# Performance work log

Measured on AMD Instinct MI355X. Metric: run time of the kernel, lower is better.

## Reference

```python
import jax, jax.numpy as jnp
import numpy as np

N = 50000      # nodes
E = 800000     # edges (before self loops)
F_IN = 128     # dataset.num_features
HID = 32       # hidden_channels (per GAT head)
HEADS = 4
C = 40         # dataset.num_classes
NEG_SLOPE = 0.2


def setup_inputs() -> dict:
    key = jax.random.key(0)
    ks = jax.random.split(key, 18)
    g = lambda k, shape, fan: jax.random.normal(k, shape, dtype=jnp.float32) / np.sqrt(fan)
    inp = {
        "x": jax.random.normal(ks[0], (N, F_IN), dtype=jnp.float32),
        "edge_index": jax.random.randint(ks[1], (2, E), 0, N, dtype=jnp.int64),
        # GAT layer 1: F_IN -> HEADS*HID
        "gat_W1": g(ks[2], (F_IN, HEADS * HID), F_IN),
        "gat_att_src1": g(ks[3], (HEADS, HID), HID),
        "gat_att_dst1": g(ks[4], (HEADS, HID), HID),
        "gat_b1": jnp.zeros((HEADS * HID,), jnp.float32),
        # GAT layer 2: HEADS*HID -> C, heads=1
        "gat_W2": g(ks[5], (HEADS * HID, C), HEADS * HID),
        "gat_att_src2": g(ks[6], (1, C), C),
        "gat_att_dst2": g(ks[7], (1, C), C),
        "gat_b2": jnp.zeros((C,), jnp.float32),
        # GCN layers
        "gcn_W1": g(ks[8], (F_IN, HID), F_IN),
        "gcn_b1": jnp.zeros((HID,), jnp.float32),
        "gcn_W2": g(ks[9], (HID, C), HID),
        "gcn_b2": jnp.zeros((C,), jnp.float32),
        # final linear: 2C -> C
        "lin_W": g(ks[10], (2 * C, C), 2 * C),
        "lin_b": jnp.zeros((C,), jnp.float32),
        "weight_c": jnp.float32(0.5),
        "weight_t": jnp.float32(0.5),
    }
    return inp


def _add_self_loops(src, dst, n):
    loop = jnp.arange(n, dtype=src.dtype)
    return jnp.concatenate([src, loop]), jnp.concatenate([dst, loop])


def _gat_conv(x, src, dst, n, W, att_src, att_dst, b, heads, out_dim):
    # h: [n, heads, out_dim]
    h = (x @ W).reshape(n, heads, out_dim)
    a_s = jnp.einsum('nhd,hd->nh', h, att_src)   # source-side attention logit
    a_d = jnp.einsum('nhd,hd->nh', h, att_dst)   # target-side attention logit
    e = jax.nn.leaky_relu(a_s[src] + a_d[dst], NEG_SLOPE)  # [E', heads]
    # softmax over incoming edges of each target node (self loops guarantee >=1 edge)
    m = jax.ops.segment_max(e, dst, num_segments=n)
    ex = jnp.exp(e - m[dst])
    s = jax.ops.segment_sum(ex, dst, num_segments=n)
    alpha = ex / s[dst]                          # [E', heads]
    out = jax.ops.segment_sum(h[src] * alpha[..., None], dst, num_segments=n)
    return out.reshape(n, heads * out_dim) + b


def _gcn_conv(x, src, dst, n, W, b):
    h = x @ W
    deg = jax.ops.segment_sum(jnp.ones(src.shape, h.dtype), dst, num_segments=n)
    norm = jax.lax.rsqrt(deg)                    # deg >= 1 (self loops)
    coef = (norm[src] * norm[dst])[:, None]
    return jax.ops.segment_sum(h[src] * coef, dst, num_segments=n) + b


def reference(x, edge_index, gat_W1, gat_att_src1, gat_att_dst1, gat_b1,
              gat_W2, gat_att_src2, gat_att_dst2, gat_b2,
              gcn_W1, gcn_b1, gcn_W2, gcn_b2, lin_W, lin_b,
              weight_c, weight_t):
    n = x.shape[0]
    src, dst = _add_self_loops(edge_index[0], edge_index[1], n)
    # GAT branch (dropout is identity at inference)
    x_gat = _gat_conv(x, src, dst, n, gat_W1, gat_att_src1, gat_att_dst1,
                      gat_b1, HEADS, HID)
    x_gat = jax.nn.elu(x_gat)
    x_gat = _gat_conv(x_gat, src, dst, n, gat_W2, gat_att_src2, gat_att_dst2,
                      gat_b2, 1, C)
    # GCN branch
    x_gcn = jax.nn.relu(_gcn_conv(x, src, dst, n, gcn_W1, gcn_b1))
    x_gcn = _gcn_conv(x_gcn, src, dst, n, gcn_W2, gcn_b2)
    # weighted feature concat + linear head
    cat = jnp.concatenate([x_gcn * weight_c, x_gat * weight_t], axis=1)  # [n, 2C]
    return cat @ lin_W + lin_b
```

## Files before the change

### kernel.cpp

```cpp
#include <hip/hip_runtime.h>
#include <math.h>

#define F_IN   128
#define HIDC   32
#define NHEAD  4
#define CDIM   40
#define NEG_SLOPE 0.2f
#define BCAP   4096
#define OVCAP  16384
#define SCHUNK 4096

typedef __attribute__((ext_vector_type(8))) short bf16x8;
typedef __attribute__((ext_vector_type(4))) float f32x4;

__device__ __forceinline__ float leakyf(float x) { return x > 0.f ? x : NEG_SLOPE * x; }

__device__ __forceinline__ float sel4(float4 v, int h) {
    return (h == 0) ? v.x : (h == 1) ? v.y : (h == 2) ? v.z : v.w;
}
__device__ __forceinline__ unsigned pack2_bf16(float a, float b) {
    unsigned ua = __float_as_uint(a);
    unsigned ub = __float_as_uint(b);
    ua = (ua + 0x7FFFu + ((ua >> 16) & 1u)) >> 16;
    ub = (ub + 0x7FFFu + ((ub >> 16) & 1u)) >> 16;
    return ua | (ub << 16);
}
__device__ __forceinline__ float2 unpack2_bf16(unsigned p) {
    return make_float2(__uint_as_float(p << 16), __uint_as_float(p & 0xFFFF0000u));
}

__global__ void wb_prep_kernel(const float* __restrict__ Wg, const float* __restrict__ Wc,
                               uint4* __restrict__ wbf)
{
    int b = blockIdx.x;
    int lane = threadIdx.x;
    int nt = b >> 2, ks = b & 3;
    int c = nt * 16 + (lane & 15);
    int k0 = ks * 32 + (lane >> 4) * 8;
    unsigned u[4];
#pragma unroll
    for (int jj = 0; jj < 4; ++jj) {
        int k = k0 + 2 * jj;
        float a0 = (c < 128) ? Wg[(size_t)k * 128 + c] : Wc[(size_t)k * 32 + (c - 128)];
        float a1 = (c < 128) ? Wg[(size_t)(k + 1) * 128 + c] : Wc[(size_t)(k + 1) * 32 + (c - 128)];
        u[jj] = pack2_bf16(a0, a1);
    }
    wbf[(size_t)b * 64 + lane] = make_uint4(u[0], u[1], u[2], u[3]);
}

__global__ __launch_bounds__(256) void gemm1_mfma_kernel(
    const float* __restrict__ X, const uint4* __restrict__ wbf,
    const float* __restrict__ aw_s, const float* __restrict__ aw_d,
    unsigned* __restrict__ hb,
    float* __restrict__ as1, float* __restrict__ ad1, int n)
{
    __shared__ float Ct[64][164];
    __shared__ float sw[128], dw[128];
    const int tid = threadIdx.x;
    const int w = tid >> 6, lane = tid & 63;
    const int m = lane & 15, q = lane >> 4;
    const int node0 = blockIdx.x * 64;
    if (tid < 128) { sw[tid] = aw_s[tid]; dw[tid] = aw_d[tid]; }

    f32x4 acc[10];
#pragma unroll
    for (int t = 0; t < 10; ++t) acc[t] = (f32x4){0.f, 0.f, 0.f, 0.f};

    const int row = node0 + w * 16 + m;
    const bool rv = row < n;
#pragma unroll
    for (int ks = 0; ks < 4; ++ks) {
        uint4 pa = make_uint4(0u, 0u, 0u, 0u);
        if (rv) {
            const float* xr = X + (size_t)row * 128 + ks * 32 + q * 8;
            float4 a0 = *(const float4*)xr;
            float4 a1 = *(const float4*)(xr + 4);
            pa = make_uint4(pack2_bf16(a0.x, a0.y), pack2_bf16(a0.z, a0.w),
                            pack2_bf16(a1.x, a1.y), pack2_bf16(a1.z, a1.w));
        }
        bf16x8 af = *(bf16x8*)&pa;
#pragma unroll
        for (int nt = 0; nt < 10; ++nt) {
            uint4 pb = wbf[(size_t)(nt * 4 + ks) * 64 + lane];
            bf16x8 bfv = *(bf16x8*)&pb;
            acc[nt] = __builtin_amdgcn_mfma_f32_16x16x32_bf16(af, bfv, acc[nt], 0, 0, 0);
        }
    }
#pragma unroll
    for (int nt = 0; nt < 10; ++nt)
#pragma unroll
        for (int r = 0; r < 4; ++r)
            Ct[w * 16 + q * 4 + r][nt * 16 + m] = acc[nt][r];
    __syncthreads();

    for (int i = tid; i < 64 * 64; i += 256) {
        int nd = i >> 6, u = i & 63;
        int gn = node0 + nd;
        if (gn < n)
            hb[(size_t)gn * 80 + u] = pack2_bf16(Ct[nd][2 * u], Ct[nd][2 * u + 1]);
    }
    for (int i = tid; i < 64 * 16; i += 256) {
        int nd = i >> 4, u = i & 15;
        int gn = node0 + nd;
        if (gn < n)
            hb[(size_t)gn * 80 + 64 + u] = pack2_bf16(Ct[nd][128 + 2 * u], Ct[nd][128 + 2 * u + 1]);
    }
    {
        int nd = tid >> 2, h = tid & 3;
        int gn = node0 + nd;
        if (gn < n) {
            float s = 0.f, d = 0.f;
#pragma unroll
            for (int k = 0; k < HIDC; ++k) {
                float v = Ct[nd][h * HIDC + k];
                s = fmaf(v, sw[h * HIDC + k], s);
                d = fmaf(v, dw[h * HIDC + k], d);
            }
            as1[(size_t)gn * 4 + h] = s;
            ad1[(size_t)gn * 4 + h] = d;
        }
    }
}

template<int K, int OUTC, int BN, int BK, int OSTRIDE = OUTC>
__global__ __launch_bounds__((OUTC / 4) * (BN / 4)) void gemm_tile(
    const float* __restrict__ X, const float* __restrict__ W,
    const float* __restrict__ bias, float* __restrict__ Y, int n)
{
    constexpr int CG = OUTC / 4;
    constexpr int NG = BN / 4;
    constexpr int NT = CG * NG;
    __shared__ float Xs[BK][BN + 4];
    __shared__ float Ws[BK][OUTC];
    const int tid = threadIdx.x;
    const int cg = tid % CG, ng = tid / CG;
    const int node0 = blockIdx.x * BN;
    float acc[4][4] = {};

    for (int kb = 0; kb < K; kb += BK) {
        for (int idx = tid; idx < BN * (BK / 4); idx += NT) {
            int nd = idx / (BK / 4);
            int kq = idx % (BK / 4);
            int gnode = node0 + nd;
            float4 v = (gnode < n) ? *(const float4*)&X[(size_t)gnode * K + kb + kq * 4]
                                   : make_float4(0.f, 0.f, 0.f, 0.f);
            Xs[kq * 4 + 0][nd] = v.x;
            Xs[kq * 4 + 1][nd] = v.y;
            Xs[kq * 4 + 2][nd] = v.z;
            Xs[kq * 4 + 3][nd] = v.w;
        }
        for (int idx = tid; idx < BK * CG; idx += NT) {
            int kk = idx / CG;
            int cq = idx % CG;
            *(float4*)&Ws[kk][cq * 4] = *(const float4*)&W[(size_t)(kb + kk) * OUTC + cq * 4];
        }
        __syncthreads();
#pragma unroll
        for (int k = 0; k < BK; ++k) {
            float4 xv = *(const float4*)&Xs[k][ng * 4];
            float4 wv = *(const float4*)&Ws[k][cg * 4];
            float xa[4] = {xv.x, xv.y, xv.z, xv.w};
            float wa[4] = {wv.x, wv.y, wv.z, wv.w};
#pragma unroll
            for (int j = 0; j < 4; ++j)
#pragma unroll
                for (int c = 0; c < 4; ++c)
                    acc[j][c] = fmaf(xa[j], wa[c], acc[j][c]);
        }
        __syncthreads();
    }

    float4 bv = make_float4(0.f, 0.f, 0.f, 0.f);
    if (bias) bv = *(const float4*)&bias[cg * 4];
#pragma unroll
    for (int j = 0; j < 4; ++j) {
        int gnode = node0 + ng * 4 + j;
        if (gnode < n) {
            float4 o = make_float4(acc[j][0] + bv.x, acc[j][1] + bv.y,
                                   acc[j][2] + bv.z, acc[j][3] + bv.w);
            *(float4*)&Y[(size_t)gnode * OSTRIDE + cg * 4] = o;
        }
    }
}

template<int K, int OUTC, int BN, int BK, int OSTRIDE_U, int OFF_U>
__global__ __launch_bounds__((OUTC / 4) * (BN / 4)) void gemm_tile_bb(
    const unsigned* __restrict__ Xb, const float* __restrict__ W,
    unsigned* __restrict__ Yb, int n)
{
    constexpr int CG = OUTC / 4;
    constexpr int NG = BN / 4;
    constexpr int NT = CG * NG;
    __shared__ float Xs[BK][BN + 4];
    __shared__ float Ws[BK][OUTC];
    const int tid = threadIdx.x;
    const int cg = tid % CG, ng = tid / CG;
    const int node0 = blockIdx.x * BN;
    float acc[4][4] = {};

    for (int kb = 0; kb < K; kb += BK) {
        for (int idx = tid; idx < BN * (BK / 8); idx += NT) {
            int nd = idx / (BK / 8);
            int kq = idx % (BK / 8);
            int gnode = node0 + nd;
            uint4 v = (gnode < n) ? *(const uint4*)&Xb[(size_t)gnode * (K / 2) + kb / 2 + kq * 4]
                                  : make_uint4(0u, 0u, 0u, 0u);
            float2 a = unpack2_bf16(v.x), b = unpack2_bf16(v.y);
            float2 c = unpack2_bf16(v.z), d = unpack2_bf16(v.w);
            Xs[kq * 8 + 0][nd] = a.x; Xs[kq * 8 + 1][nd] = a.y;
            Xs[kq * 8 + 2][nd] = b.x; Xs[kq * 8 + 3][nd] = b.y;
            Xs[kq * 8 + 4][nd] = c.x; Xs[kq * 8 + 5][nd] = c.y;
            Xs[kq * 8 + 6][nd] = d.x; Xs[kq * 8 + 7][nd] = d.y;
        }
        for (int idx = tid; idx < BK * CG; idx += NT) {
            int kk = idx / CG;
            int cq = idx % CG;
            *(float4*)&Ws[kk][cq * 4] = *(const float4*)&W[(size_t)(kb + kk) * OUTC + cq * 4];
        }
        __syncthreads();
#pragma unroll
        for (int k = 0; k < BK; ++k) {
            float4 xv = *(const float4*)&Xs[k][ng * 4];
            float4 wv = *(const float4*)&Ws[k][cg * 4];
            float xa[4] = {xv.x, xv.y, xv.z, xv.w};
            float wa[4] = {wv.x, wv.y, wv.z, wv.w};
#pragma unroll
            for (int j = 0; j < 4; ++j)
#pragma unroll
                for (int c = 0; c < 4; ++c)
                    acc[j][c] = fmaf(xa[j], wa[c], acc[j][c]);
        }
        __syncthreads();
    }

#pragma unroll
    for (int j = 0; j < 4; ++j) {
        int gnode = node0 + ng * 4 + j;
        if (gnode < n) {
            uint2 pb = make_uint2(pack2_bf16(acc[j][0], acc[j][1]),
                                  pack2_bf16(acc[j][2], acc[j][3]));
            *(uint2*)&Yb[(size_t)gnode * OSTRIDE_U + OFF_U + cg * 2] = pb;
        }
    }
}

__global__ __launch_bounds__(320) void gemm2_gat_kernel(
    const unsigned* __restrict__ Xb, const float* __restrict__ W,
    const float* __restrict__ aw_s, const float* __restrict__ aw_d,
    unsigned* __restrict__ Yb, float* __restrict__ as2, float* __restrict__ ad2, int n)
{
    constexpr int K = 128, OUTC = 40, BN = 128, BK = 32;
    constexpr int CG = OUTC / 4, NT = 320;
    __shared__ float smem[32 * 132 + 32 * 40];
    float* Xs = smem;
    float* Ws = smem + 32 * 132;
    const int tid = threadIdx.x;
    const int cg = tid % CG, ng = tid / CG;
    const int node0 = blockIdx.x * BN;
    float acc[4][4] = {};

    for (int kb = 0; kb < K; kb += BK) {
        for (int idx = tid; idx < BN * (BK / 8); idx += NT) {
            int nd = idx / (BK / 8);
            int kq = idx % (BK / 8);
            int gnode = node0 + nd;
            uint4 v = (gnode < n) ? *(const uint4*)&Xb[(size_t)gnode * (K / 2) + kb / 2 + kq * 4]
                                  : make_uint4(0u, 0u, 0u, 0u);
            float2 a = unpack2_bf16(v.x), b = unpack2_bf16(v.y);
            float2 c = unpack2_bf16(v.z), d = unpack2_bf16(v.w);
            Xs[(kq * 8 + 0) * 132 + nd] = a.x; Xs[(kq * 8 + 1) * 132 + nd] = a.y;
            Xs[(kq * 8 + 2) * 132 + nd] = b.x; Xs[(kq * 8 + 3) * 132 + nd] = b.y;
            Xs[(kq * 8 + 4) * 132 + nd] = c.x; Xs[(kq * 8 + 5) * 132 + nd] = c.y;
            Xs[(kq * 8 + 6) * 132 + nd] = d.x; Xs[(kq * 8 + 7) * 132 + nd] = d.y;
        }
        for (int idx = tid; idx < BK * CG; idx += NT) {
            int kk = idx / CG;
            int cq = idx % CG;
            *(float4*)&Ws[kk * 40 + cq * 4] = *(const float4*)&W[(size_t)(kb + kk) * OUTC + cq * 4];
        }
        __syncthreads();
#pragma unroll
        for (int k = 0; k < BK; ++k) {
            float4 xv = *(const float4*)&Xs[k * 132 + ng * 4];
            float4 wv = *(const float4*)&Ws[k * 40 + cg * 4];
            float xa[4] = {xv.x, xv.y, xv.z, xv.w};
            float wa[4] = {wv.x, wv.y, wv.z, wv.w};
#pragma unroll
            for (int j = 0; j < 4; ++j)
#pragma unroll
                for (int c = 0; c < 4; ++c)
                    acc[j][c] = fmaf(xa[j], wa[c], acc[j][c]);
        }
        __syncthreads();
    }

    float* Ct  = smem;
    float* sww = smem + 128 * 41;
    float* dww = sww + 40;
#pragma unroll
    for (int j = 0; j < 4; ++j) {
        int gnode = node0 + ng * 4 + j;
        if (gnode < n) {
            uint2 pb = make_uint2(pack2_bf16(acc[j][0], acc[j][1]),
                                  pack2_bf16(acc[j][2], acc[j][3]));
            *(uint2*)&Yb[(size_t)gnode * 40 + cg * 2] = pb;
        }
#pragma unroll
        for (int c = 0; c < 4; ++c)
            Ct[(ng * 4 + j) * 41 + cg * 4 + c] = acc[j][c];
    }
    if (tid < 40) { sww[tid] = aw_s[tid]; dww[tid] = aw_d[tid]; }
    __syncthreads();
    if (tid < 128) {
        int gnode = node0 + tid;
        if (gnode < n) {
            float s = 0.f, d = 0.f;
#pragma unroll
            for (int c = 0; c < 40; ++c) {
                float v = Ct[tid * 41 + c];
                s = fmaf(v, sww[c], s);
                d = fmaf(v, dww[c], d);
            }
            as2[gnode] = s;
            ad2[gnode] = d;
        }
    }
}

__global__ __launch_bounds__(256) void bucket_scatter_kernel(
    const int* __restrict__ src, const int* __restrict__ dst,
    unsigned* __restrict__ bcnt, unsigned* __restrict__ bpair,
    unsigned* __restrict__ ovf_cnt, uint2* __restrict__ ovf, int e, int nbuck)
{
    __shared__ unsigned hist[512];
    __shared__ unsigned base[512];
    const int t = threadIdx.x;
    const int lo = blockIdx.x * SCHUNK;
    const int hi = min(lo + SCHUNK, e);
    for (int i = t; i < nbuck; i += 256) hist[i] = 0;
    __syncthreads();
    for (int i = lo + t; i < hi; i += 256)
        atomicAdd(&hist[((unsigned)dst[i]) >> 7], 1u);
    __syncthreads();
    for (int i = t; i < nbuck; i += 256) {
        unsigned c = hist[i];
        base[i] = c ? atomicAdd(&bcnt[i], c) : 0u;
        hist[i] = 0;
    }
    __syncthreads();
    for (int i = lo + t; i < hi; i += 256) {
        unsigned s = (unsigned)src[i], d = (unsigned)dst[i];
        unsigned b = d >> 7;
        unsigned pos = base[b] + atomicAdd(&hist[b], 1u);
        if (pos < BCAP) bpair[(size_t)b * BCAP + pos] = s | ((d & 127u) << 16);
        else {
            unsigned o = atomicAdd(ovf_cnt, 1u);
            if (o < OVCAP) ovf[o] = make_uint2(s, d);
        }
    }
}

__global__ __launch_bounds__(256) void bucket_count_kernel(
    const unsigned* __restrict__ bcnt, const unsigned* __restrict__ bpair,
    const unsigned* __restrict__ ovf_cnt, const uint2* __restrict__ ovf,
    unsigned* __restrict__ counts, int n)
{
    __shared__ unsigned lc[128];
    const int b = blockIdx.x, base = b << 7;
    if (threadIdx.x < 128) lc[threadIdx.x] = 0;
    __syncthreads();
    unsigned bc = bcnt[b];
    int cnt = (int)(bc < BCAP ? bc : BCAP);
    for (int k = threadIdx.x; k < cnt; k += 256)
        atomicAdd(&lc[bpair[(size_t)b * BCAP + k] >> 16], 1u);
    unsigned oc_u = *ovf_cnt;
    int oc = (int)(oc_u < OVCAP ? oc_u : OVCAP);
    for (int k = threadIdx.x; k < oc; k += 256) {
        uint2 pp = ovf[k];
        if ((int)(pp.y >> 7) == b) atomicAdd(&lc[pp.y & 127u], 1u);
    }
    __syncthreads();
    int i = base + threadIdx.x;
    if (threadIdx.x < 128 && i < n) counts[i] = lc[threadIdx.x];
}

__global__ __launch_bounds__(256) void scan_reduce_kernel(const unsigned* __restrict__ counts,
                                                          unsigned* __restrict__ partials, int n)
{
    __shared__ unsigned sm[256];
    int t = threadIdx.x;
    int i = blockIdx.x * 256 + t;
    unsigned v = (i < n) ? counts[i] : 0u;
    sm[t] = v;
    __syncthreads();
#pragma unroll
    for (int off = 128; off > 0; off >>= 1) {
        if (t < off) sm[t] += sm[t + off];
        __syncthreads();
    }
    if (t == 0) partials[blockIdx.x] = sm[0];
}

__global__ __launch_bounds__(256) void scan_partials_kernel(unsigned* __restrict__ partials,
                                                            unsigned* __restrict__ rs, int nb, int n)
{
    __shared__ unsigned sm[256];
    int t = threadIdx.x;
    unsigned v = (t < nb) ? partials[t] : 0u;
    sm[t] = v;
    __syncthreads();
#pragma unroll
    for (int off = 1; off < 256; off <<= 1) {
        unsigned u = (t >= off) ? sm[t - off] : 0u;
        __syncthreads();
        sm[t] += u;
        __syncthreads();
    }
    if (t < nb) partials[t] = sm[t] - v;
    if (t == 255) rs[n] = sm[255];
}

__global__ __launch_bounds__(256) void scan_write_kernel(const unsigned* __restrict__ counts,
                                                         const unsigned* __restrict__ partials,
                                                         unsigned* __restrict__ rs,
                                                         float* __restrict__ nrm, int n)
{
    __shared__ unsigned sm[256];
    int t = threadIdx.x;
    int i = blockIdx.x * 256 + t;
    unsigned c = (i < n) ? counts[i] : 0u;
    sm[t] = c;
    __syncthreads();
#pragma unroll
    for (int off = 1; off < 256; off <<= 1) {
        unsigned u = (t >= off) ? sm[t - off] : 0u;
        __syncthreads();
        sm[t] += u;
        __syncthreads();
    }
    if (i < n) {
        rs[i] = partials[blockIdx.x] + sm[t] - c;
        nrm[i] = rsqrtf((float)(c + 1u));
    }
}

__global__ __launch_bounds__(256) void bucket_place_kernel(
    const unsigned* __restrict__ bcnt, const unsigned* __restrict__ bpair,
    const unsigned* __restrict__ rs, unsigned* __restrict__ csr_src,
    unsigned* __restrict__ cursor, int n)
{
    __shared__ unsigned lc[128];
    __shared__ unsigned rbase[128];
    const int b = blockIdx.x, base = b << 7;
    if (threadIdx.x < 128) {
        lc[threadIdx.x] = 0;
        int i = base + threadIdx.x;
        rbase[threadIdx.x] = (i < n) ? rs[i] : 0u;
    }
    __syncthreads();
    unsigned bc = bcnt[b];
    int cnt = (int)(bc < BCAP ? bc : BCAP);
    for (int k = threadIdx.x; k < cnt; k += 256) {
        unsigned v = bpair[(size_t)b * BCAP + k];
        unsigned ld = v >> 16;
        unsigned r = atomicAdd(&lc[ld], 1u);
        csr_src[rbase[ld] + r] = v & 0xFFFFu;
    }
    __syncthreads();
    int i = base + threadIdx.x;
    if (threadIdx.x < 128 && i < n) cursor[i] = rbase[threadIdx.x] + lc[threadIdx.x];
}

__global__ void overflow_fill_kernel(const unsigned* __restrict__ ovf_cnt,
                                     const uint2* __restrict__ ovf,
                                     unsigned* __restrict__ cursor,
                                     unsigned* __restrict__ csr_src)
{
    unsigned oc_u = *ovf_cnt;
    int oc = (int)(oc_u < OVCAP ? oc_u : OVCAP);
    for (int k = threadIdx.x; k < oc; k += 256) {
        uint2 pp = ovf[k];
        unsigned pos = atomicAdd(&cursor[pp.y], 1u);
        csr_src[pos] = pp.x;
    }
}

__global__ __launch_bounds__(256) void agg1_fused_kernel(
    const unsigned* __restrict__ hb,
    const float* __restrict__ as1, const float* __restrict__ ad1,
    const float* __restrict__ nrm,
    const unsigned* __restrict__ rs, const unsigned* __restrict__ csr_src,
    const float* __restrict__ gat_b1, const float* __restrict__ gcn_b1,
    unsigned* __restrict__ xgb, unsigned* __restrict__ gaccb, int n)
{
    const int wid = threadIdx.x >> 6;
    const int lane = threadIdx.x & 63;
    const int i = blockIdx.x * 4 + wid;
    if (i >= n) return;
    const unsigned beg = rs[i];
    const int deg = (int)(rs[i + 1] - beg);
    const float4* as1v = (const float4*)as1;
    const uint4*  hv4  = (const uint4*)hb;

    const int e = lane >> 4, c = lane & 15;
    const int h = c >> 2;
    const bool gc = c < 4;

    const float4 dv = ((const float4*)ad1)[i];
    const float dvh = sel4(dv, h);
    const float ni  = nrm[i];

    unsigned pre = (lane < deg) ? csr_src[beg + lane] : (unsigned)i;

    const float4 av = as1v[i];
    const float eself = __expf(leakyf(sel4(av, h) + dvh));

    float acc[8], gacc[8];
#pragma unroll
    for (int t = 0; t < 8; ++t) { acc[t] = 0.f; gacc[t] = 0.f; }
    float sumw = 0.f;

    if (e == 0) {
        uint4 hv = hv4[(size_t)i * 20 + c];
        float2 p0 = unpack2_bf16(hv.x), p1 = unpack2_bf16(hv.y);
        float2 p2 = unpack2_bf16(hv.z), p3 = unpack2_bf16(hv.w);
        acc[0] = p0.x * eself; acc[1] = p0.y * eself;
        acc[2] = p1.x * eself; acc[3] = p1.y * eself;
        acc[4] = p2.x * eself; acc[5] = p2.y * eself;
        acc[6] = p3.x * eself; acc[7] = p3.y * eself;
        if (gc) {
            uint4 gv = hv4[(size_t)i * 20 + 16 + c];
            float w2s = ni * ni;
            float2 q0 = unpack2_bf16(gv.x), q1 = unpack2_bf16(gv.y);
            float2 q2 = unpack2_bf16(gv.z), q3 = unpack2_bf16(gv.w);
            gacc[0] = q0.x * w2s; gacc[1] = q0.y * w2s;
            gacc[2] = q1.x * w2s; gacc[3] = q1.y * w2s;
            gacc[4] = q2.x * w2s; gacc[5] = q2.y * w2s;
            gacc[6] = q3.x * w2s; gacc[7] = q3.y * w2s;
        }
    }

    const int dfast = deg < 64 ? deg : 64;
    const int steps = (dfast + 3) >> 2;

    float4 a_cur = make_float4(0.f, 0.f, 0.f, 0.f);
    uint4  h_cur = make_uint4(0u, 0u, 0u, 0u);
    uint4  g_cur = make_uint4(0u, 0u, 0u, 0u);
    float  nr_cur = 0.f;
    if (steps > 0) {
        unsigned s = __shfl(pre, e, 64);
        if (e >= deg) s = (unsigned)i;
        a_cur = as1v[s];
        h_cur = hv4[(size_t)s * 20 + c];
        if (gc) { g_cur = hv4[(size_t)s * 20 + 16 + c]; nr_cur = nrm[s]; }
    }
    for (int j = 0; j < steps; ++j) {
        float4 a_nxt = a_cur;
        uint4  h_nxt = h_cur, g_nxt = g_cur;
        float  nr_nxt = nr_cur;
        if (j + 1 < steps) {
            int idx = (j + 1) * 4 + e;
            unsigned s = __shfl(pre, idx, 64);
            if (idx >= deg) s = (unsigned)i;
            a_nxt = as1v[s];
            h_nxt = hv4[(size_t)s * 20 + c];
            if (gc) { g_nxt = hv4[(size_t)s * 20 + 16 + c]; nr_nxt = nrm[s]; }
        }
        const bool val = (j * 4 + e) < deg;
        float w = __expf(leakyf(sel4(a_cur, h) + dvh));
        w = val ? w : 0.f;
        sumw += w;
        {
            float2 p0 = unpack2_bf16(h_cur.x), p1 = unpack2_bf16(h_cur.y);
            float2 p2 = unpack2_bf16(h_cur.z), p3 = unpack2_bf16(h_cur.w);
            acc[0] = fmaf(p0.x, w, acc[0]); acc[1] = fmaf(p0.y, w, acc[1]);
            acc[2] = fmaf(p1.x, w, acc[2]); acc[3] = fmaf(p1.y, w, acc[3]);
            acc[4] = fmaf(p2.x, w, acc[4]); acc[5] = fmaf(p2.y, w, acc[5]);
            acc[6] = fmaf(p3.x, w, acc[6]); acc[7] = fmaf(p3.y, w, acc[7]);
        }
        if (gc) {
            float cw = val ? nr_cur * ni : 0.f;
            float2 q0 = unpack2_bf16(g_cur.x), q1 = unpack2_bf16(g_cur.y);
            float2 q2 = unpack2_bf16(g_cur.z), q3 = unpack2_bf16(g_cur.w);
            gacc[0] = fmaf(q0.x, cw, gacc[0]); gacc[1] = fmaf(q0.y, cw, gacc[1]);
            gacc[2] = fmaf(q1.x, cw, gacc[2]); gacc[3] = fmaf(q1.y, cw, gacc[3]);
            gacc[4] = fmaf(q2.x, cw, gacc[4]); gacc[5] = fmaf(q2.y, cw, gacc[5]);
            gacc[6] = fmaf(q3.x, cw, gacc[6]); gacc[7] = fmaf(q3.y, cw, gacc[7]);
        }
        a_cur = a_nxt; h_cur = h_nxt; g_cur = g_nxt; nr_cur = nr_nxt;
    }
    for (int j4 = 64; j4 < deg; j4 += 4) {
        int idx = j4 + e;
        bool val = idx < deg;
        unsigned s = val ? csr_src[beg + idx] : (unsigned)i;
        float4 a = as1v[s];
        float w = val ? __expf(leakyf(sel4(a, h) + dvh)) : 0.f;
        sumw += w;
        uint4 hv = hv4[(size_t)s * 20 + c];
        float2 p0 = unpack2_bf16(hv.x), p1 = unpack2_bf16(hv.y);
        float2 p2 = unpack2_bf16(hv.z), p3 = unpack2_bf16(hv.w);
        acc[0] = fmaf(p0.x, w, acc[0]); acc[1] = fmaf(p0.y, w, acc[1]);
        acc[2] = fmaf(p1.x, w, acc[2]); acc[3] = fmaf(p1.y, w, acc[3]);
        acc[4] = fmaf(p2.x, w, acc[4]); acc[5] = fmaf(p2.y, w, acc[5]);
        acc[6] = fmaf(p3.x, w, acc[6]); acc[7] = fmaf(p3.y, w, acc[7]);
        if (gc) {
            float cw = val ? nrm[s] * ni : 0.f;
            uint4 gv = hv4[(size_t)s * 20 + 16 + c];
            float2 q0 = unpack2_bf16(gv.x), q1 = unpack2_bf16(gv.y);
            float2 q2 = unpack2_bf16(gv.z), q3 = unpack2_bf16(gv.w);
            gacc[0] = fmaf(q0.x, cw, gacc[0]); gacc[1] = fmaf(q0.y, cw, gacc[1]);
            gacc[2] = fmaf(q1.x, cw, gacc[2]); gacc[3] = fmaf(q1.y, cw, gacc[3]);
            gacc[4] = fmaf(q2.x, cw, gacc[4]); gacc[5] = fmaf(q2.y, cw, gacc[5]);
            gacc[6] = fmaf(q3.x, cw, gacc[6]); gacc[7] = fmaf(q3.y, cw, gacc[7]);
        }
    }

#pragma unroll
    for (int t = 0; t < 8; ++t) {
        acc[t]  += __shfl_xor(acc[t], 16, 64);
        acc[t]  += __shfl_xor(acc[t], 32, 64);
        gacc[t] += __shfl_xor(gacc[t], 16, 64);
        gacc[t] += __shfl_xor(gacc[t], 32, 64);
    }
    sumw += __shfl_xor(sumw, 16, 64);
    sumw += __shfl_xor(sumw, 32, 64);
    const float ssh = sumw + eself;

    if (e == 0) {
        float inv = 1.f / ssh;
        float4 b0 = *(const float4*)&gat_b1[c * 8];
        float4 b1 = *(const float4*)&gat_b1[c * 8 + 4];
        float o[8] = {acc[0] * inv + b0.x, acc[1] * inv + b0.y,
                      acc[2] * inv + b0.z, acc[3] * inv + b0.w,
                      acc[4] * inv + b1.x, acc[5] * inv + b1.y,
                      acc[6] * inv + b1.z, acc[7] * inv + b1.w};
#pragma unroll
        for (int t = 0; t < 8; ++t) o[t] = o[t] > 0.f ? o[t] : __expf(o[t]) - 1.f;
        uint4 pv = make_uint4(pack2_bf16(o[0], o[1]), pack2_bf16(o[2], o[3]),
                              pack2_bf16(o[4], o[5]), pack2_bf16(o[6], o[7]));
        ((uint4*)xgb)[(size_t)i * 16 + c] = pv;
        if (gc) {
            float4 c0 = *(const float4*)&gcn_b1[c * 8];
            float4 c1 = *(const float4*)&gcn_b1[c * 8 + 4];
            float g[8] = {fmaxf(gacc[0] + c0.x, 0.f), fmaxf(gacc[1] + c0.y, 0.f),
                          fmaxf(gacc[2] + c0.z, 0.f), fmaxf(gacc[3] + c0.w, 0.f),
                          fmaxf(gacc[4] + c1.x, 0.f), fmaxf(gacc[5] + c1.y, 0.f),
                          fmaxf(gacc[6] + c1.z, 0.f), fmaxf(gacc[7] + c1.w, 0.f)};
            uint4 gv = make_uint4(pack2_bf16(g[0], g[1]), pack2_bf16(g[2], g[3]),
                                  pack2_bf16(g[4], g[5]), pack2_bf16(g[6], g[7]));
            ((uint4*)gaccb)[(size_t)i * 4 + c] = gv;
        }
    }
}

__global__ __launch_bounds__(256) void agg2_fused_kernel(
    const unsigned* __restrict__ hg_b, const float* __restrict__ as2,
    const float* __restrict__ ad2, const float* __restrict__ nrm,
    const unsigned* __restrict__ rs, const unsigned* __restrict__ csr_src,
    const float* __restrict__ gat_b2, const float* __restrict__ gcn_b2,
    const float* __restrict__ wc_p, const float* __restrict__ wt_p,
    float* __restrict__ cat, int n)
{
    const int wid = threadIdx.x >> 6;
    const int lane = threadIdx.x & 63;
    const int i = blockIdx.x * 4 + wid;
    if (i >= n) return;
    const unsigned beg = rs[i];
    const int deg = (int)(rs[i + 1] - beg);
    const int e = lane & 3, c = lane >> 2;
    const bool act = c < 10, isgat = c < 5;
    const float adv = ad2[i];
    const float ni = nrm[i];
    const uint4* hgv = (const uint4*)hg_b;

    unsigned pre = (lane < deg) ? csr_src[beg + lane] : (unsigned)i;
    const float eself = __expf(leakyf(as2[i] + adv));

    float acc[8];
#pragma unroll
    for (int t = 0; t < 8; ++t) acc[t] = 0.f;
    float sumw = 0.f;

    if (act && e == 0) {
        uint4 hv = hgv[(size_t)i * 10 + c];
        float sw = isgat ? eself : ni * ni;
        float2 p0 = unpack2_bf16(hv.x), p1 = unpack2_bf16(hv.y);
        float2 p2 = unpack2_bf16(hv.z), p3 = unpack2_bf16(hv.w);
        acc[0] = p0.x * sw; acc[1] = p0.y * sw;
        acc[2] = p1.x * sw; acc[3] = p1.y * sw;
        acc[4] = p2.x * sw; acc[5] = p2.y * sw;
        acc[6] = p3.x * sw; acc[7] = p3.y * sw;
    }

    const int dfast = deg < 64 ? deg : 64;
    const int steps = (dfast + 3) >> 2;

    float aw_cur = 0.f;
    uint4 h_cur = make_uint4(0u, 0u, 0u, 0u);
    if (steps > 0) {
        unsigned s = __shfl(pre, e, 64);
        if (e >= deg) s = (unsigned)i;
        if (act) { aw_cur = isgat ? as2[s] : nrm[s]; h_cur = hgv[(size_t)s * 10 + c]; }
    }
    for (int j = 0; j < steps; ++j) {
        float aw_nxt = aw_cur;
        uint4 h_nxt = h_cur;
        if (j + 1 < steps) {
            int idx = (j + 1) * 4 + e;
            unsigned s = __shfl(pre, idx, 64);
            if (idx >= deg) s = (unsigned)i;
            if (act) { aw_nxt = isgat ? as2[s] : nrm[s]; h_nxt = hgv[(size_t)s * 10 + c]; }
        }
        const bool val = (j * 4 + e) < deg;
        float w;
        if (isgat) {
            w = __expf(leakyf(aw_cur + adv));
            w = val ? w : 0.f;
            sumw += w;
        } else {
            w = val ? aw_cur * ni : 0.f;
        }
        if (act) {
            float2 p0 = unpack2_bf16(h_cur.x), p1 = unpack2_bf16(h_cur.y);
            float2 p2 = unpack2_bf16(h_cur.z), p3 = unpack2_bf16(h_cur.w);
            acc[0] = fmaf(p0.x, w, acc[0]); acc[1] = fmaf(p0.y, w, acc[1]);
            acc[2] = fmaf(p1.x, w, acc[2]); acc[3] = fmaf(p1.y, w, acc[3]);
            acc[4] = fmaf(p2.x, w, acc[4]); acc[5] = fmaf(p2.y, w, acc[5]);
            acc[6] = fmaf(p3.x, w, acc[6]); acc[7] = fmaf(p3.y, w, acc[7]);
        }
        aw_cur = aw_nxt; h_cur = h_nxt;
    }
    for (int j4 = 64; j4 < deg; j4 += 4) {
        int idx = j4 + e;
        bool val = idx < deg;
        unsigned s = val ? csr_src[beg + idx] : (unsigned)i;
        if (act) {
            float aw = isgat ? as2[s] : nrm[s];
            float w;
            if (isgat) {
                w = val ? __expf(leakyf(aw + adv)) : 0.f;
                sumw += w;
            } else {
                w = val ? aw * ni : 0.f;
            }
            uint4 hv = hgv[(size_t)s * 10 + c];
            float2 p0 = unpack2_bf16(hv.x), p1 = unpack2_bf16(hv.y);
            float2 p2 = unpack2_bf16(hv.z), p3 = unpack2_bf16(hv.w);
            acc[0] = fmaf(p0.x, w, acc[0]); acc[1] = fmaf(p0.y, w, acc[1]);
            acc[2] = fmaf(p1.x, w, acc[2]); acc[3] = fmaf(p1.y, w, acc[3]);
            acc[4] = fmaf(p2.x, w, acc[4]); acc[5] = fmaf(p2.y, w, acc[5]);
            acc[6] = fmaf(p3.x, w, acc[6]); acc[7] = fmaf(p3.y, w, acc[7]);
        }
    }

#pragma unroll
    for (int t = 0; t < 8; ++t) {
        acc[t] += __shfl_xor(acc[t], 1, 64);
        acc[t] += __shfl_xor(acc[t], 2, 64);
    }
    sumw += __shfl_xor(sumw, 1, 64);
    sumw += __shfl_xor(sumw, 2, 64);
    const float ssum = sumw + eself;

    if (act && e == 0) {
        if (isgat) {
            float inv = 1.f / ssum, wt = *wt_p;
            float4 b0 = *(const float4*)&gat_b2[c * 8];
            float4 b1 = *(const float4*)&gat_b2[c * 8 + 4];
            float4 o0 = make_float4((acc[0] * inv + b0.x) * wt, (acc[1] * inv + b0.y) * wt,
                                    (acc[2] * inv + b0.z) * wt, (acc[3] * inv + b0.w) * wt);
            float4 o1 = make_float4((acc[4] * inv + b1.x) * wt, (acc[5] * inv + b1.y) * wt,
                                    (acc[6] * inv + b1.z) * wt, (acc[7] * inv + b1.w) * wt);
            *(float4*)&cat[(size_t)i * 80 + 40 + c * 8]     = o0;
            *(float4*)&cat[(size_t)i * 80 + 40 + c * 8 + 4] = o1;
        } else {
            float wc = *wc_p;
            int g = c - 5;
            float4 b0 = *(const float4*)&gcn_b2[g * 8];
            float4 b1 = *(const float4*)&gcn_b2[g * 8 + 4];
            float4 o0 = make_float4((acc[0] + b0.x) * wc, (acc[1] + b0.y) * wc,
                                    (acc[2] + b0.z) * wc, (acc[3] + b0.w) * wc);
            float4 o1 = make_float4((acc[4] + b1.x) * wc, (acc[5] + b1.y) * wc,
                                    (acc[6] + b1.z) * wc, (acc[7] + b1.w) * wc);
            *(float4*)&cat[(size_t)i * 80 + g * 8]     = o0;
            *(float4*)&cat[(size_t)i * 80 + g * 8 + 4] = o1;
        }
    }
}

extern "C" void kernel_launch(void* const* d_in, const int* in_sizes, int n_in,
                              void* d_out, int out_size, void* d_ws, size_t ws_size,
                              hipStream_t stream)
{
    const float* x        = (const float*)d_in[0];
    const int*   eidx     = (const int*)d_in[1];
    const float* gat_W1   = (const float*)d_in[2];
    const float* att_s1   = (const float*)d_in[3];
    const float* att_d1   = (const float*)d_in[4];
    const float* gat_b1   = (const float*)d_in[5];
    const float* gat_W2   = (const float*)d_in[6];
    const float* att_s2   = (const float*)d_in[7];
    const float* att_d2   = (const float*)d_in[8];
    const float* gat_b2   = (const float*)d_in[9];
    const float* gcn_W1   = (const float*)d_in[10];
    const float* gcn_b1   = (const float*)d_in[11];
    const float* gcn_W2   = (const float*)d_in[12];
    const float* gcn_b2   = (const float*)d_in[13];
    const float* lin_W    = (const float*)d_in[14];
    const float* lin_b    = (const float*)d_in[15];
    const float* wc_p     = (const float*)d_in[16];
    const float* wt_p     = (const float*)d_in[17];

    const int n = in_sizes[0] / F_IN;
    const int e = in_sizes[1] / 2;
    const int* src = eidx;
    const int* dst = eidx + e;
    const int NBUCK = (n + 127) >> 7;

    char* p = (char*)d_ws;
    auto alloc = [&](size_t bytes) -> void* {
        void* r = (void*)p;
        p += (bytes + 255) & ~(size_t)255;
        return r;
    };
    unsigned* counts  = (unsigned*)alloc((size_t)n * 4);
    unsigned* rs      = (unsigned*)alloc((size_t)(n + 1) * 4);
    unsigned* cursor  = (unsigned*)alloc((size_t)n * 4);
    unsigned* partials= (unsigned*)alloc(256 * 4);
    unsigned* bcnt    = (unsigned*)alloc((size_t)(NBUCK + 1) * 4);
    unsigned* csr_src = (unsigned*)alloc((size_t)e * 4);
    uint4*    wbf     = (uint4*)alloc(40 * 64 * 16);
    float* nrm     = (float*)alloc((size_t)n * 4);
    float* as1     = (float*)alloc((size_t)n * 4 * 4);
    float* ad1     = (float*)alloc((size_t)n * 4 * 4);
    float* as2     = (float*)alloc((size_t)n * 4);
    float* ad2     = (float*)alloc((size_t)n * 4);
    float* cat     = (float*)alloc((size_t)n * 80 * 4);
    unsigned* hg_b = (unsigned*)alloc((size_t)n * 40 * 4);
    float* xg      = (float*)alloc((size_t)n * F_IN * 4);
    unsigned* gaccb= (unsigned*)alloc((size_t)n * 16 * 4);
    unsigned* bpair = (unsigned*)cat;
    uint2*    ovf   = (uint2*)(bpair + (size_t)NBUCK * BCAP);
    unsigned* hb    = (unsigned*)cat;
    unsigned* xgb   = (unsigned*)xg;
    unsigned* ovf_cnt = bcnt + NBUCK;

    const int NB = (n + 255) / 256;
    const int WB = (n + 3) / 4;
    const int SB = (e + SCHUNK - 1) / SCHUNK;

    hipMemsetAsync(bcnt, 0, (size_t)(NBUCK + 1) * 4, stream);
    bucket_scatter_kernel<<<SB, 256, 0, stream>>>(src, dst, bcnt, bpair, ovf_cnt, ovf, e, NBUCK);
    bucket_count_kernel<<<NBUCK, 256, 0, stream>>>(bcnt, bpair, ovf_cnt, ovf, counts, n);
    scan_reduce_kernel<<<NB, 256, 0, stream>>>(counts, partials, n);
    scan_partials_kernel<<<1, 256, 0, stream>>>(partials, rs, NB, n);
    scan_write_kernel<<<NB, 256, 0, stream>>>(counts, partials, rs, nrm, n);
    bucket_place_kernel<<<NBUCK, 256, 0, stream>>>(bcnt, bpair, rs, csr_src, cursor, n);
    overflow_fill_kernel<<<1, 256, 0, stream>>>(ovf_cnt, ovf, cursor, csr_src);

    wb_prep_kernel<<<40, 64, 0, stream>>>(gat_W1, gcn_W1, wbf);
    gemm1_mfma_kernel<<<(n + 63) / 64, 256, 0, stream>>>(x, wbf, att_s1, att_d1,
                                                         hb, as1, ad1, n);

    agg1_fused_kernel<<<WB, 256, 0, stream>>>(hb, as1, ad1, nrm, rs, csr_src,
                                              gat_b1, gcn_b1, xgb, gaccb, n);

    gemm_tile_bb<32, 40, 128, 32, 40, 20><<<(n + 127) / 128, 320, 0, stream>>>(gaccb, gcn_W2, hg_b, n);
    gemm2_gat_kernel<<<(n + 127) / 128, 320, 0, stream>>>(xgb, gat_W2, att_s2, att_d2,
                                                          hg_b, as2, ad2, n);

    agg2_fused_kernel<<<WB, 256, 0, stream>>>(hg_b, as2, ad2, nrm, rs, csr_src,
                                              gat_b2, gcn_b2, wc_p, wt_p, cat, n);

    gemm_tile<80, 40, 128, 40><<<(n + 127) / 128, 320, 0, stream>>>(cat, lin_W, lin_b, (float*)d_out, n);
}
```

Measured before the change: 306.0 us.

## Process two nodes per wavefront in aggregations and fuse final linear into agg2

Both aggregation kernels now handle two destination nodes per wavefront, interleaving their gathers so each wave keeps more independent memory requests in flight. The final linear layer is folded into agg2: the concatenated features are combined in registers via lane shuffles and multiplied by the transposed weights, removing the cat buffer round-trip and a separate GEMM launch. The cost is higher register pressure, and wasted work when the two nodes' degrees differ.

```diff
diff --git a/kernel.cpp b/kernel.cpp
--- a/kernel.cpp
+++ b/kernel.cpp
@@ -118,67 +118,6 @@
             }
             as1[(size_t)gn * 4 + h] = s;
             ad1[(size_t)gn * 4 + h] = d;
-        }
-    }
-}
-
-template<int K, int OUTC, int BN, int BK, int OSTRIDE = OUTC>
-__global__ __launch_bounds__((OUTC / 4) * (BN / 4)) void gemm_tile(
-    const float* __restrict__ X, const float* __restrict__ W,
-    const float* __restrict__ bias, float* __restrict__ Y, int n)
-{
-    constexpr int CG = OUTC / 4;
-    constexpr int NG = BN / 4;
-    constexpr int NT = CG * NG;
-    __shared__ float Xs[BK][BN + 4];
-    __shared__ float Ws[BK][OUTC];
-    const int tid = threadIdx.x;
-    const int cg = tid % CG, ng = tid / CG;
-    const int node0 = blockIdx.x * BN;
-    float acc[4][4] = {};
-
-    for (int kb = 0; kb < K; kb += BK) {
-        for (int idx = tid; idx < BN * (BK / 4); idx += NT) {
-            int nd = idx / (BK / 4);
-            int kq = idx % (BK / 4);
-            int gnode = node0 + nd;
-            float4 v = (gnode < n) ? *(const float4*)&X[(size_t)gnode * K + kb + kq * 4]
-                                   : make_float4(0.f, 0.f, 0.f, 0.f);
-            Xs[kq * 4 + 0][nd] = v.x;
-            Xs[kq * 4 + 1][nd] = v.y;
-            Xs[kq * 4 + 2][nd] = v.z;
-            Xs[kq * 4 + 3][nd] = v.w;
-        }
-        for (int idx = tid; idx < BK * CG; idx += NT) {
-            int kk = idx / CG;
-            int cq = idx % CG;
-            *(float4*)&Ws[kk][cq * 4] = *(const float4*)&W[(size_t)(kb + kk) * OUTC + cq * 4];
-        }
-        __syncthreads();
-#pragma unroll
-        for (int k = 0; k < BK; ++k) {
-            float4 xv = *(const float4*)&Xs[k][ng * 4];
-            float4 wv = *(const float4*)&Ws[k][cg * 4];
-            float xa[4] = {xv.x, xv.y, xv.z, xv.w};
-            float wa[4] = {wv.x, wv.y, wv.z, wv.w};
-#pragma unroll
-            for (int j = 0; j < 4; ++j)
-#pragma unroll
-                for (int c = 0; c < 4; ++c)
-                    acc[j][c] = fmaf(xa[j], wa[c], acc[j][c]);
-        }
-        __syncthreads();
-    }
-
-    float4 bv = make_float4(0.f, 0.f, 0.f, 0.f);
-    if (bias) bv = *(const float4*)&bias[cg * 4];
-#pragma unroll
-    for (int j = 0; j < 4; ++j) {
-        int gnode = node0 + ng * 4 + j;
-        if (gnode < n) {
-            float4 o = make_float4(acc[j][0] + bv.x, acc[j][1] + bv.y,
-                                   acc[j][2] + bv.z, acc[j][3] + bv.w);
-            *(float4*)&Y[(size_t)gnode * OSTRIDE + cg * 4] = o;
         }
     }
 }
@@ -495,160 +434,263 @@
 {
     const int wid = threadIdx.x >> 6;
     const int lane = threadIdx.x & 63;
-    const int i = blockIdx.x * 4 + wid;
-    if (i >= n) return;
-    const unsigned beg = rs[i];
-    const int deg = (int)(rs[i + 1] - beg);
+    const int iA = blockIdx.x * 8 + wid * 2;
+    if (iA >= n) return;
+    const int iB = iA + 1;
+    const bool hasB = iB < n;
+    const int iBs = hasB ? iB : iA;
+
     const float4* as1v = (const float4*)as1;
+    const float4* ad1v = (const float4*)ad1;
     const uint4*  hv4  = (const uint4*)hb;
 
     const int e = lane >> 4, c = lane & 15;
     const int h = c >> 2;
     const bool gc = c < 4;
 
-    const float4 dv = ((const float4*)ad1)[i];
-    const float dvh = sel4(dv, h);
-    const float ni  = nrm[i];
-
-    unsigned pre = (lane < deg) ? csr_src[beg + lane] : (unsigned)i;
-
-    const float4 av = as1v[i];
-    const float eself = __expf(leakyf(sel4(av, h) + dvh));
-
-    float acc[8], gacc[8];
-#pragma unroll
-    for (int t = 0; t < 8; ++t) { acc[t] = 0.f; gacc[t] = 0.f; }
-    float sumw = 0.f;
+    const unsigned begA = rs[iA];
+    const int degA = (int)(rs[iA + 1] - begA);
+    const unsigned begB = rs[iBs];
+    const int degB = hasB ? (int)(rs[iB + 1] - begB) : 0;
+
+    const float dvhA = sel4(ad1v[iA], h);
+    const float dvhB = sel4(ad1v[iBs], h);
+    const float niA = nrm[iA];
+    const float niB = nrm[iBs];
+
+    unsigned preA = (lane < degA) ? csr_src[begA + lane] : (unsigned)iA;
+    unsigned preB = (lane < degB) ? csr_src[begB + lane] : (unsigned)iBs;
+
+    const float eselfA = __expf(leakyf(sel4(as1v[iA], h) + dvhA));
+    const float eselfB = __expf(leakyf(sel4(as1v[iBs], h) + dvhB));
+
+    float accA[8], gaccA[8], accB[8], gaccB[8];
+#pragma unroll
+    for (int t = 0; t < 8; ++t) { accA[t] = 0.f; gaccA[t] = 0.f; accB[t] = 0.f; gaccB[t] = 0.f; }
+    float sumwA = 0.f, sumwB = 0.f;
 
     if (e == 0) {
-        uint4 hv = hv4[(size_t)i * 20 + c];
+        uint4 hv = hv4[(size_t)iA * 20 + c];
         float2 p0 = unpack2_bf16(hv.x), p1 = unpack2_bf16(hv.y);
         float2 p2 = unpack2_bf16(hv.z), p3 = unpack2_bf16(hv.w);
-        acc[0] = p0.x * eself; acc[1] = p0.y * eself;
-        acc[2] = p1.x * eself; acc[3] = p1.y * eself;
-        acc[4] = p2.x * eself; acc[5] = p2.y * eself;
-        acc[6] = p3.x * eself; acc[7] = p3.y * eself;
+        accA[0] = p0.x * eselfA; accA[1] = p0.y * eselfA;
+        accA[2] = p1.x * eselfA; accA[3] = p1.y * eselfA;
+        accA[4] = p2.x * eselfA; accA[5] = p2.y * eselfA;
+        accA[6] = p3.x * eselfA; accA[7] = p3.y * eselfA;
         if (gc) {
-            uint4 gv = hv4[(size_t)i * 20 + 16 + c];
-            float w2s = ni * ni;
+            uint4 gv = hv4[(size_t)iA * 20 + 16 + c];
+            float w2 = niA * niA;
             float2 q0 = unpack2_bf16(gv.x), q1 = unpack2_bf16(gv.y);
             float2 q2 = unpack2_bf16(gv.z), q3 = unpack2_bf16(gv.w);
-            gacc[0] = q0.x * w2s; gacc[1] = q0.y * w2s;
-            gacc[2] = q1.x * w2s; gacc[3] = q1.y * w2s;
-            gacc[4] = q2.x * w2s; gacc[5] = q2.y * w2s;
-            gacc[6] = q3.x * w2s; gacc[7] = q3.y * w2s;
-        }
-    }
-
-    const int dfast = deg < 64 ? deg : 64;
-    const int steps = (dfast + 3) >> 2;
-
-    float4 a_cur = make_float4(0.f, 0.f, 0.f, 0.f);
-    uint4  h_cur = make_uint4(0u, 0u, 0u, 0u);
-    uint4  g_cur = make_uint4(0u, 0u, 0u, 0u);
-    float  nr_cur = 0.f;
+            gaccA[0] = q0.x * w2; gaccA[1] = q0.y * w2;
+            gaccA[2] = q1.x * w2; gaccA[3] = q1.y * w2;
+            gaccA[4] = q2.x * w2; gaccA[5] = q2.y * w2;
+            gaccA[6] = q3.x * w2; gaccA[7] = q3.y * w2;
+        }
+    }
+    if (e == 1 && hasB) {
+        uint4 hv = hv4[(size_t)iB * 20 + c];
+        float2 p0 = unpack2_bf16(hv.x), p1 = unpack2_bf16(hv.y);
+        float2 p2 = unpack2_bf16(hv.z), p3 = unpack2_bf16(hv.w);
+        accB[0] = p0.x * eselfB; accB[1] = p0.y * eselfB;
+        accB[2] = p1.x * eselfB; accB[3] = p1.y * eselfB;
+        accB[4] = p2.x * eselfB; accB[5] = p2.y * eselfB;
+        accB[6] = p3.x * eselfB; accB[7] = p3.y * eselfB;
+        if (gc) {
+            uint4 gv = hv4[(size_t)iB * 20 + 16 + c];
+            float w2 = niB * niB;
+            float2 q0 = unpack2_bf16(gv.x), q1 = unpack2_bf16(gv.y);
+            float2 q2 = unpack2_bf16(gv.z), q3 = unpack2_bf16(gv.w);
+            gaccB[0] = q0.x * w2; gaccB[1] = q0.y * w2;
+            gaccB[2] = q1.x * w2; gaccB[3] = q1.y * w2;
+            gaccB[4] = q2.x * w2; gaccB[5] = q2.y * w2;
+            gaccB[6] = q3.x * w2; gaccB[7] = q3.y * w2;
+        }
+    }
+
+    const int dA = degA < 64 ? degA : 64;
+    const int dB = degB < 64 ? degB : 64;
+    const int stepsA = (dA + 3) >> 2;
+    const int stepsB = (dB + 3) >> 2;
+    const int steps = stepsA > stepsB ? stepsA : stepsB;
+
+    auto fetch = [&](unsigned pre, int deg, int selfi, int idx,
+                     float4& a, uint4& hh, uint4& gg, float& nr) {
+        unsigned s = __shfl(pre, idx, 64);
+        if (idx >= deg) s = (unsigned)selfi;
+        a = as1v[s];
+        hh = hv4[(size_t)s * 20 + c];
+        if (gc) { gg = hv4[(size_t)s * 20 + 16 + c]; nr = nrm[s]; }
+    };
+
+    float4 aA = make_float4(0.f, 0.f, 0.f, 0.f), aB = aA;
+    uint4 hA = make_uint4(0u, 0u, 0u, 0u), hB = hA, gA = hA, gB = hA;
+    float nrA = 0.f, nrB = 0.f;
     if (steps > 0) {
-        unsigned s = __shfl(pre, e, 64);
-        if (e >= deg) s = (unsigned)i;
-        a_cur = as1v[s];
-        h_cur = hv4[(size_t)s * 20 + c];
-        if (gc) { g_cur = hv4[(size_t)s * 20 + 16 + c]; nr_cur = nrm[s]; }
+        fetch(preA, degA, iA, e, aA, hA, gA, nrA);
+        fetch(preB, degB, iBs, e, aB, hB, gB, nrB);
     }
     for (int j = 0; j < steps; ++j) {
-        float4 a_nxt = a_cur;
-        uint4  h_nxt = h_cur, g_nxt = g_cur;
-        float  nr_nxt = nr_cur;
+        float4 aA2 = aA, aB2 = aB;
+        uint4 hA2 = hA, hB2 = hB, gA2 = gA, gB2 = gB;
+        float nrA2 = nrA, nrB2 = nrB;
         if (j + 1 < steps) {
-            int idx = (j + 1) * 4 + e;
-            unsigned s = __shfl(pre, idx, 64);
-            if (idx >= deg) s = (unsigned)i;
-            a_nxt = as1v[s];
-            h_nxt = hv4[(size_t)s * 20 + c];
-            if (gc) { g_nxt = hv4[(size_t)s * 20 + 16 + c]; nr_nxt = nrm[s]; }
-        }
-        const bool val = (j * 4 + e) < deg;
-        float w = __expf(leakyf(sel4(a_cur, h) + dvh));
-        w = val ? w : 0.f;
-        sumw += w;
+            fetch(preA, degA, iA, (j + 1) * 4 + e, aA2, hA2, gA2, nrA2);
+            fetch(preB, degB, iBs, (j + 1) * 4 + e, aB2, hB2, gB2, nrB2);
+        }
         {
-            float2 p0 = unpack2_bf16(h_cur.x), p1 = unpack2_bf16(h_cur.y);
-            float2 p2 = unpack2_bf16(h_cur.z), p3 = unpack2_bf16(h_cur.w);
-            acc[0] = fmaf(p0.x, w, acc[0]); acc[1] = fmaf(p0.y, w, acc[1]);
-            acc[2] = fmaf(p1.x, w, acc[2]); acc[3] = fmaf(p1.y, w, acc[3]);
-            acc[4] = fmaf(p2.x, w, acc[4]); acc[5] = fmaf(p2.y, w, acc[5]);
-            acc[6] = fmaf(p3.x, w, acc[6]); acc[7] = fmaf(p3.y, w, acc[7]);
-        }
-        if (gc) {
-            float cw = val ? nr_cur * ni : 0.f;
-            float2 q0 = unpack2_bf16(g_cur.x), q1 = unpack2_bf16(g_cur.y);
-            float2 q2 = unpack2_bf16(g_cur.z), q3 = unpack2_bf16(g_cur.w);
-            gacc[0] = fmaf(q0.x, cw, gacc[0]); gacc[1] = fmaf(q0.y, cw, gacc[1]);
-            gacc[2] = fmaf(q1.x, cw, gacc[2]); gacc[3] = fmaf(q1.y, cw, gacc[3]);
-            gacc[4] = fmaf(q2.x, cw, gacc[4]); gacc[5] = fmaf(q2.y, cw, gacc[5]);
-            gacc[6] = fmaf(q3.x, cw, gacc[6]); gacc[7] = fmaf(q3.y, cw, gacc[7]);
-        }
-        a_cur = a_nxt; h_cur = h_nxt; g_cur = g_nxt; nr_cur = nr_nxt;
-    }
-    for (int j4 = 64; j4 < deg; j4 += 4) {
+            const bool val = (j * 4 + e) < degA;
+            float w = __expf(leakyf(sel4(aA, h) + dvhA));
+            w = val ? w : 0.f;
+            sumwA += w;
+            float2 p0 = unpack2_bf16(hA.x), p1 = unpack2_bf16(hA.y);
+            float2 p2 = unpack2_bf16(hA.z), p3 = unpack2_bf16(hA.w);
+            accA[0] = fmaf(p0.x, w, accA[0]); accA[1] = fmaf(p0.y, w, accA[1]);
+            accA[2] = fmaf(p1.x, w, accA[2]); accA[3] = fmaf(p1.y, w, accA[3]);
+            accA[4] = fmaf(p2.x, w, accA[4]); accA[5] = fmaf(p2.y, w, accA[5]);
+            accA[6] = fmaf(p3.x, w, accA[6]); accA[7] = fmaf(p3.y, w, accA[7]);
+            if (gc) {
+                float cw = val ? nrA * niA : 0.f;
+                float2 q0 = unpack2_bf16(gA.x), q1 = unpack2_bf16(gA.y);
+                float2 q2 = unpack2_bf16(gA.z), q3 = unpack2_bf16(gA.w);
+                gaccA[0] = fmaf(q0.x, cw, gaccA[0]); gaccA[1] = fmaf(q0.y, cw, gaccA[1]);
+                gaccA[2] = fmaf(q1.x, cw, gaccA[2]); gaccA[3] = fmaf(q1.y, cw, gaccA[3]);
+                gaccA[4] = fmaf(q2.x, cw, gaccA[4]); gaccA[5] = fmaf(q2.y, cw, gaccA[5]);
+                gaccA[6] = fmaf(q3.x, cw, gaccA[6]); gaccA[7] = fmaf(q3.y, cw, gaccA[7]);
+            }
+        }
+        {
+            const bool val = (j * 4 + e) < degB;
+            float w = __expf(leakyf(sel4(aB, h) + dvhB));
+            w = val ? w : 0.f;
+            sumwB += w;
+            float2 p0 = unpack2_bf16(hB.x), p1 = unpack2_bf16(hB.y);
+            float2 p2 = unpack2_bf16(hB.z), p3 = unpack2_bf16(hB.w);
+            accB[0] = fmaf(p0.x, w, accB[0]); accB[1] = fmaf(p0.y, w, accB[1]);
+            accB[2] = fmaf(p1.x, w, accB[2]); accB[3] = fmaf(p1.y, w, accB[3]);
+            accB[4] = fmaf(p2.x, w, accB[4]); accB[5] = fmaf(p2.y, w, accB[5]);
+            accB[6] = fmaf(p3.x, w, accB[6]); accB[7] = fmaf(p3.y, w, accB[7]);
+            if (gc) {
+                float cw = val ? nrB * niB : 0.f;
+                float2 q0 = unpack2_bf16(gB.x), q1 = unpack2_bf16(gB.y);
+                float2 q2 = unpack2_bf16(gB.z), q3 = unpack2_bf16(gB.w);
+                gaccB[0] = fmaf(q0.x, cw, gaccB[0]); gaccB[1] = fmaf(q0.y, cw, gaccB[1]);
+                gaccB[2] = fmaf(q1.x, cw, gaccB[2]); gaccB[3] = fmaf(q1.y, cw, gaccB[3]);
+                gaccB[4] = fmaf(q2.x, cw, gaccB[4]); gaccB[5] = fmaf(q2.y, cw, gaccB[5]);
+                gaccB[6] = fmaf(q3.x, cw, gaccB[6]); gaccB[7] = fmaf(q3.y, cw, gaccB[7]);
+            }
+        }
+        aA = aA2; aB = aB2; hA = hA2; hB = hB2; gA = gA2; gB = gB2; nrA = nrA2; nrB = nrB2;
+    }
+    for (int j4 = 64; j4 < degA; j4 += 4) {
         int idx = j4 + e;
-        bool val = idx < deg;
-        unsigned s = val ? csr_src[beg + idx] : (unsigned)i;
-        float4 a = as1v[s];
-        float w = val ? __expf(leakyf(sel4(a, h) + dvh)) : 0.f;
-        sumw += w;
+        bool val = idx < degA;
+        unsigned s = val ? csr_src[begA + idx] : (unsigned)iA;
+        float w = val ? __expf(leakyf(sel4(as1v[s], h) + dvhA)) : 0.f;
+        sumwA += w;
         uint4 hv = hv4[(size_t)s * 20 + c];
         float2 p0 = unpack2_bf16(hv.x), p1 = unpack2_bf16(hv.y);
         float2 p2 = unpack2_bf16(hv.z), p3 = unpack2_bf16(hv.w);
-        acc[0] = fmaf(p0.x, w, acc[0]); acc[1] = fmaf(p0.y, w, acc[1]);
-        acc[2] = fmaf(p1.x, w, acc[2]); acc[3] = fmaf(p1.y, w, acc[3]);
-        acc[4] = fmaf(p2.x, w, acc[4]); acc[5] = fmaf(p2.y, w, acc[5]);
-        acc[6] = fmaf(p3.x, w, acc[6]); acc[7] = fmaf(p3.y, w, acc[7]);
+        accA[0] = fmaf(p0.x, w, accA[0]); accA[1] = fmaf(p0.y, w, accA[1]);
+        accA[2] = fmaf(p1.x, w, accA[2]); accA[3] = fmaf(p1.y, w, accA[3]);
+        accA[4] = fmaf(p2.x, w, accA[4]); accA[5] = fmaf(p2.y, w, accA[5]);
+        accA[6] = fmaf(p3.x, w, accA[6]); accA[7] = fmaf(p3.y, w, accA[7]);
         if (gc) {
-            float cw = val ? nrm[s] * ni : 0.f;
+            float cw = val ? nrm[s] * niA : 0.f;
             uint4 gv = hv4[(size_t)s * 20 + 16 + c];
             float2 q0 = unpack2_bf16(gv.x), q1 = unpack2_bf16(gv.y);
             float2 q2 = unpack2_bf16(gv.z), q3 = unpack2_bf16(gv.w);
-            gacc[0] = fmaf(q0.x, cw, gacc[0]); gacc[1] = fmaf(q0.y, cw, gacc[1]);
-            gacc[2] = fmaf(q1.x, cw, gacc[2]); gacc[3] = fmaf(q1.y, cw, gacc[3]);
-            gacc[4] = fmaf(q2.x, cw, gacc[4]); gacc[5] = fmaf(q2.y, cw, gacc[5]);
-            gacc[6] = fmaf(q3.x, cw, gacc[6]); gacc[7] = fmaf(q3.y, cw, gacc[7]);
+            gaccA[0] = fmaf(q0.x, cw, gaccA[0]); gaccA[1] = fmaf(q0.y, cw, gaccA[1]);
+            gaccA[2] = fmaf(q1.x, cw, gaccA[2]); gaccA[3] = fmaf(q1.y, cw, gaccA[3]);
+            gaccA[4] = fmaf(q2.x, cw, gaccA[4]); gaccA[5] = fmaf(q2.y, cw, gaccA[5]);
+            gaccA[6] = fmaf(q3.x, cw, gaccA[6]); gaccA[7] = fmaf(q3.y, cw, gaccA[7]);
+        }
+    }
+    for (int j4 = 64; j4 < degB; j4 += 4) {
+        int idx = j4 + e;
+        bool val = idx < degB;
+        unsigned s = val ? csr_src[begB + idx] : (unsigned)iBs;
+        float w = val ? __expf(leakyf(sel4(as1v[s], h) + dvhB)) : 0.f;
+        sumwB += w;
+        uint4 hv = hv4[(size_t)s * 20 + c];
+        float2 p0 = unpack2_bf16(hv.x), p1 = unpack2_bf16(hv.y);
+        float2 p2 = unpack2_bf16(hv.z), p3 = unpack2_bf16(hv.w);
+        accB[0] = fmaf(p0.x, w, accB[0]); accB[1] = fmaf(p0.y, w, accB[1]);
+        accB[2] = fmaf(p1.x, w, accB[2]); accB[3] = fmaf(p1.y, w, accB[3]);
+        accB[4] = fmaf(p2.x, w, accB[4]); accB[5] = fmaf(p2.y, w, accB[5]);
+        accB[6] = fmaf(p3.x, w, accB[6]); accB[7] = fmaf(p3.y, w, accB[7]);
+        if (gc) {
+            float cw = val ? nrm[s] * niB : 0.f;
+            uint4 gv = hv4[(size_t)s * 20 + 16 + c];
+            float2 q0 = unpack2_bf16(gv.x), q1 = unpack2_bf16(gv.y);
+            float2 q2 = unpack2_bf16(gv.z), q3 = unpack2_bf16(gv.w);
+            gaccB[0] = fmaf(q0.x, cw, gaccB[0]); gaccB[1] = fmaf(q0.y, cw, gaccB[1]);
+            gaccB[2] = fmaf(q1.x, cw, gaccB[2]); gaccB[3] = fmaf(q1.y, cw, gaccB[3]);
+            gaccB[4] = fmaf(q2.x, cw, gaccB[4]); gaccB[5] = fmaf(q2.y, cw, gaccB[5]);
+            gaccB[6] = fmaf(q3.x, cw, gaccB[6]); gaccB[7] = fmaf(q3.y, cw, gaccB[7]);
         }
     }
 
 #pragma unroll
     for (int t = 0; t < 8; ++t) {
-        acc[t]  += __shfl_xor(acc[t], 16, 64);
-        acc[t]  += __shfl_xor(acc[t], 32, 64);
-        gacc[t] += __shfl_xor(gacc[t], 16, 64);
-        gacc[t] += __shfl_xor(gacc[t], 32, 64);
-    }
-    sumw += __shfl_xor(sumw, 16, 64);
-    sumw += __shfl_xor(sumw, 32, 64);
-    const float ssh = sumw + eself;
+        accA[t]  += __shfl_xor(accA[t], 16, 64);  accA[t]  += __shfl_xor(accA[t], 32, 64);
+        accB[t]  += __shfl_xor(accB[t], 16, 64);  accB[t]  += __shfl_xor(accB[t], 32, 64);
+        gaccA[t] += __shfl_xor(gaccA[t], 16, 64); gaccA[t] += __shfl_xor(gaccA[t], 32, 64);
+        gaccB[t] += __shfl_xor(gaccB[t], 16, 64); gaccB[t] += __shfl_xor(gaccB[t], 32, 64);
+    }
+    sumwA += __shfl_xor(sumwA, 16, 64); sumwA += __shfl_xor(sumwA, 32, 64);
+    sumwB += __shfl_xor(sumwB, 16, 64); sumwB += __shfl_xor(sumwB, 32, 64);
+    const float sshA = sumwA + eselfA;
+    const float sshB = sumwB + eselfB;
 
     if (e == 0) {
-        float inv = 1.f / ssh;
+        float inv = 1.f / sshA;
         float4 b0 = *(const float4*)&gat_b1[c * 8];
         float4 b1 = *(const float4*)&gat_b1[c * 8 + 4];
-        float o[8] = {acc[0] * inv + b0.x, acc[1] * inv + b0.y,
-                      acc[2] * inv + b0.z, acc[3] * inv + b0.w,
-                      acc[4] * inv + b1.x, acc[5] * inv + b1.y,
-                      acc[6] * inv + b1.z, acc[7] * inv + b1.w};
+        float o[8] = {accA[0] * inv + b0.x, accA[1] * inv + b0.y,
+                      accA[2] * inv + b0.z, accA[3] * inv + b0.w,
+                      accA[4] * inv + b1.x, accA[5] * inv + b1.y,
+                      accA[6] * inv + b1.z, accA[7] * inv + b1.w};
 #pragma unroll
         for (int t = 0; t < 8; ++t) o[t] = o[t] > 0.f ? o[t] : __expf(o[t]) - 1.f;
         uint4 pv = make_uint4(pack2_bf16(o[0], o[1]), pack2_bf16(o[2], o[3]),
                               pack2_bf16(o[4], o[5]), pack2_bf16(o[6], o[7]));
-        ((uint4*)xgb)[(size_t)i * 16 + c] = pv;
+        ((uint4*)xgb)[(size_t)iA * 16 + c] = pv;
         if (gc) {
             float4 c0 = *(const float4*)&gcn_b1[c * 8];
             float4 c1 = *(const float4*)&gcn_b1[c * 8 + 4];
-            float g[8] = {fmaxf(gacc[0] + c0.x, 0.f), fmaxf(gacc[1] + c0.y, 0.f),
-                          fmaxf(gacc[2] + c0.z, 0.f), fmaxf(gacc[3] + c0.w, 0.f),
-                          fmaxf(gacc[4] + c1.x, 0.f), fmaxf(gacc[5] + c1.y, 0.f),
-                          fmaxf(gacc[6] + c1.z, 0.f), fmaxf(gacc[7] + c1.w, 0.f)};
+            float g[8] = {fmaxf(gaccA[0] + c0.x, 0.f), fmaxf(gaccA[1] + c0.y, 0.f),
+                          fmaxf(gaccA[2] + c0.z, 0.f), fmaxf(gaccA[3] + c0.w, 0.f),
+                          fmaxf(gaccA[4] + c1.x, 0.f), fmaxf(gaccA[5] + c1.y, 0.f),
+                          fmaxf(gaccA[6] + c1.z, 0.f), fmaxf(gaccA[7] + c1.w, 0.f)};
             uint4 gv = make_uint4(pack2_bf16(g[0], g[1]), pack2_bf16(g[2], g[3]),
                                   pack2_bf16(g[4], g[5]), pack2_bf16(g[6], g[7]));
-            ((uint4*)gaccb)[(size_t)i * 4 + c] = gv;
+            ((uint4*)gaccb)[(size_t)iA * 4 + c] = gv;
+        }
+    }
+    if (e == 1 && hasB) {
+        float inv = 1.f / sshB;
+        float4 b0 = *(const float4*)&gat_b1[c * 8];
+        float4 b1 = *(const float4*)&gat_b1[c * 8 + 4];
+        float o[8] = {accB[0] * inv + b0.x, accB[1] * inv + b0.y,
+                      accB[2] * inv + b0.z, accB[3] * inv + b0.w,
+                      accB[4] * inv + b1.x, accB[5] * inv + b1.y,
+                      accB[6] * inv + b1.z, accB[7] * inv + b1.w};
+#pragma unroll
+        for (int t = 0; t < 8; ++t) o[t] = o[t] > 0.f ? o[t] : __expf(o[t]) - 1.f;
+        uint4 pv = make_uint4(pack2_bf16(o[0], o[1]), pack2_bf16(o[2], o[3]),
+                              pack2_bf16(o[4], o[5]), pack2_bf16(o[6], o[7]));
+        ((uint4*)xgb)[(size_t)iB * 16 + c] = pv;
+        if (gc) {
+            float4 c0 = *(const float4*)&gcn_b1[c * 8];
+            float4 c1 = *(const float4*)&gcn_b1[c * 8 + 4];
+            float g[8] = {fmaxf(gaccB[0] + c0.x, 0.f), fmaxf(gaccB[1] + c0.y, 0.f),
+                          fmaxf(gaccB[2] + c0.z, 0.f), fmaxf(gaccB[3] + c0.w, 0.f),
+                          fmaxf(gaccB[4] + c1.x, 0.f), fmaxf(gaccB[5] + c1.y, 0.f),
+                          fmaxf(gaccB[6] + c1.z, 0.f), fmaxf(gaccB[7] + c1.w, 0.f)};
+            uint4 gv = make_uint4(pack2_bf16(g[0], g[1]), pack2_bf16(g[2], g[3]),
+                                  pack2_bf16(g[4], g[5]), pack2_bf16(g[6], g[7]));
+            ((uint4*)gaccb)[(size_t)iB * 4 + c] = gv;
         }
     }
 }
@@ -659,132 +701,213 @@
     const unsigned* __restrict__ rs, const unsigned* __restrict__ csr_src,
     const float* __restrict__ gat_b2, const float* __restrict__ gcn_b2,
     const float* __restrict__ wc_p, const float* __restrict__ wt_p,
-    float* __restrict__ cat, int n)
-{
-    const int wid = threadIdx.x >> 6;
-    const int lane = threadIdx.x & 63;
-    const int i = blockIdx.x * 4 + wid;
-    if (i >= n) return;
-    const unsigned beg = rs[i];
-    const int deg = (int)(rs[i + 1] - beg);
+    const float* __restrict__ lin_W, const float* __restrict__ lin_b,
+    float* __restrict__ Y, int n)
+{
+    __shared__ __align__(16) float Wt[40 * 84];
+    const int tid = threadIdx.x;
+    for (int idx = tid; idx < 3200; idx += 256) {
+        int k = idx / 40, oc = idx - k * 40;
+        Wt[oc * 84 + k] = lin_W[idx];
+    }
+    __syncthreads();
+
+    const int wid = tid >> 6;
+    const int lane = tid & 63;
+    const int iA = blockIdx.x * 8 + wid * 2;
+    if (iA >= n) return;
+    const int iB = iA + 1;
+    const bool hasB = iB < n;
+    const int iBs = hasB ? iB : iA;
+
+    const unsigned begA = rs[iA];
+    const int degA = (int)(rs[iA + 1] - begA);
+    const unsigned begB = rs[iBs];
+    const int degB = hasB ? (int)(rs[iB + 1] - begB) : 0;
+
     const int e = lane & 3, c = lane >> 2;
     const bool act = c < 10, isgat = c < 5;
-    const float adv = ad2[i];
-    const float ni = nrm[i];
+    const float advA = ad2[iA], advB = ad2[iBs];
+    const float niA = nrm[iA], niB = nrm[iBs];
     const uint4* hgv = (const uint4*)hg_b;
 
-    unsigned pre = (lane < deg) ? csr_src[beg + lane] : (unsigned)i;
-    const float eself = __expf(leakyf(as2[i] + adv));
-
-    float acc[8];
-#pragma unroll
-    for (int t = 0; t < 8; ++t) acc[t] = 0.f;
-    float sumw = 0.f;
+    unsigned preA = (lane < degA) ? csr_src[begA + lane] : (unsigned)iA;
+    unsigned preB = (lane < degB) ? csr_src[begB + lane] : (unsigned)iBs;
+    const float eselfA = __expf(leakyf(as2[iA] + advA));
+    const float eselfB = __expf(leakyf(as2[iBs] + advB));
+
+    float accA[8], accB[8];
+#pragma unroll
+    for (int t = 0; t < 8; ++t) { accA[t] = 0.f; accB[t] = 0.f; }
+    float sumwA = 0.f, sumwB = 0.f;
 
     if (act && e == 0) {
-        uint4 hv = hgv[(size_t)i * 10 + c];
-        float sw = isgat ? eself : ni * ni;
+        uint4 hv = hgv[(size_t)iA * 10 + c];
+        float sw = isgat ? eselfA : niA * niA;
         float2 p0 = unpack2_bf16(hv.x), p1 = unpack2_bf16(hv.y);
         float2 p2 = unpack2_bf16(hv.z), p3 = unpack2_bf16(hv.w);
-        acc[0] = p0.x * sw; acc[1] = p0.y * sw;
-        acc[2] = p1.x * sw; acc[3] = p1.y * sw;
-        acc[4] = p2.x * sw; acc[5] = p2.y * sw;
-        acc[6] = p3.x * sw; acc[7] = p3.y * sw;
-    }
-
-    const int dfast = deg < 64 ? deg : 64;
-    const int steps = (dfast + 3) >> 2;
-
-    float aw_cur = 0.f;
-    uint4 h_cur = make_uint4(0u, 0u, 0u, 0u);
+        accA[0] = p0.x * sw; accA[1] = p0.y * sw;
+        accA[2] = p1.x * sw; accA[3] = p1.y * sw;
+        accA[4] = p2.x * sw; accA[5] = p2.y * sw;
+        accA[6] = p3.x * sw; accA[7] = p3.y * sw;
+    }
+    if (act && e == 1 && hasB) {
+        uint4 hv = hgv[(size_t)iB * 10 + c];
+        float sw = isgat ? eselfB : niB * niB;
+        float2 p0 = unpack2_bf16(hv.x), p1 = unpack2_bf16(hv.y);
+        float2 p2 = unpack2_bf16(hv.z), p3 = unpack2_bf16(hv.w);
+        accB[0] = p0.x * sw; accB[1] = p0.y * sw;
+        accB[2] = p1.x * sw; accB[3] = p1.y * sw;
+        accB[4] = p2.x * sw; accB[5] = p2.y * sw;
+        accB[6] = p3.x * sw; accB[7] = p3.y * sw;
+    }
+
+    const int dA = degA < 64 ? degA : 64;
+    const int dB = degB < 64 ? degB : 64;
+    const int stepsA = (dA + 3) >> 2;
+    const int stepsB = (dB + 3) >> 2;
+    const int steps = stepsA > stepsB ? stepsA : stepsB;
+
+    auto fetch = [&](unsigned pre, int deg, int selfi, int idx, float& aw, uint4& hh) {
+        unsigned s = __shfl(pre, idx, 64);
+        if (idx >= deg) s = (unsigned)selfi;
+        if (act) { aw = isgat ? as2[s] : nrm[s]; hh = hgv[(size_t)s * 10 + c]; }
+    };
+
+    float awA = 0.f, awB = 0.f;
+    uint4 hA = make_uint4(0u, 0u, 0u, 0u), hB = hA;
     if (steps > 0) {
-        unsigned s = __shfl(pre, e, 64);
-        if (e >= deg) s = (unsigned)i;
-        if (act) { aw_cur = isgat ? as2[s] : nrm[s]; h_cur = hgv[(size_t)s * 10 + c]; }
+        fetch(preA, degA, iA, e, awA, hA);
+        fetch(preB, degB, iBs, e, awB, hB);
     }
     for (int j = 0; j < steps; ++j) {
-        float aw_nxt = aw_cur;
-        uint4 h_nxt = h_cur;
+        float awA2 = awA, awB2 = awB;
+        uint4 hA2 = hA, hB2 = hB;
         if (j + 1 < steps) {
-            int idx = (j + 1) * 4 + e;
-            unsigned s = __shfl(pre, idx, 64);
-            if (idx >= deg) s = (unsigned)i;
-            if (act) { aw_nxt = isgat ? as2[s] : nrm[s]; h_nxt = hgv[(size_t)s * 10 + c]; }
-        }
-        const bool val = (j * 4 + e) < deg;
-        float w;
-        if (isgat) {
-            w = __expf(leakyf(aw_cur + adv));
-            w = val ? w : 0.f;
-            sumw += w;
-        } else {
-            w = val ? aw_cur * ni : 0.f;
-        }
-        if (act) {
-            float2 p0 = unpack2_bf16(h_cur.x), p1 = unpack2_bf16(h_cur.y);
-            float2 p2 = unpack2_bf16(h_cur.z), p3 = unpack2_bf16(h_cur.w);
-            acc[0] = fmaf(p0.x, w, acc[0]); acc[1] = fmaf(p0.y, w, acc[1]);
-            acc[2] = fmaf(p1.x, w, acc[2]); acc[3] = fmaf(p1.y, w, acc[3]);
-            acc[4] = fmaf(p2.x, w, acc[4]); acc[5] = fmaf(p2.y, w, acc[5]);
-            acc[6] = fmaf(p3.x, w, acc[6]); acc[7] = fmaf(p3.y, w, acc[7]);
-        }
-        aw_cur = aw_nxt; h_cur = h_nxt;
-    }
-    for (int j4 = 64; j4 < deg; j4 += 4) {
+            fetch(preA, degA, iA, (j + 1) * 4 + e, awA2, hA2);
+            fetch(preB, degB, iBs, (j + 1) * 4 + e, awB2, hB2);
+        }
+        {
+            const bool val = (j * 4 + e) < degA;
+            float w;
+            if (isgat) { w = __expf(leakyf(awA + advA)); w = val ? w : 0.f; sumwA += w; }
+            else       { w = val ? awA * niA : 0.f; }
+            if (act) {
+                float2 p0 = unpack2_bf16(hA.x), p1 = unpack2_bf16(hA.y);
+                float2 p2 = unpack2_bf16(hA.z), p3 = unpack2_bf16(hA.w);
+                accA[0] = fmaf(p0.x, w, accA[0]); accA[1] = fmaf(p0.y, w, accA[1]);
+                accA[2] = fmaf(p1.x, w, accA[2]); accA[3] = fmaf(p1.y, w, accA[3]);
+                accA[4] = fmaf(p2.x, w, accA[4]); accA[5] = fmaf(p2.y, w, accA[5]);
+                accA[6] = fmaf(p3.x, w, accA[6]); accA[7] = fmaf(p3.y, w, accA[7]);
+            }
+        }
+        {
+            const bool val = (j * 4 + e) < degB;
+            float w;
+            if (isgat) { w = __expf(leakyf(awB + advB)); w = val ? w : 0.f; sumwB += w; }
+            else       { w = val ? awB * niB : 0.f; }
+            if (act) {
+                float2 p0 = unpack2_bf16(hB.x), p1 = unpack2_bf16(hB.y);
+                float2 p2 = unpack2_bf16(hB.z), p3 = unpack2_bf16(hB.w);
+                accB[0] = fmaf(p0.x, w, accB[0]); accB[1] = fmaf(p0.y, w, accB[1]);
+                accB[2] = fmaf(p1.x, w, accB[2]); accB[3] = fmaf(p1.y, w, accB[3]);
+                accB[4] = fmaf(p2.x, w, accB[4]); accB[5] = fmaf(p2.y, w, accB[5]);
+                accB[6] = fmaf(p3.x, w, accB[6]); accB[7] = fmaf(p3.y, w, accB[7]);
+            }
+        }
+        awA = awA2; awB = awB2; hA = hA2; hB = hB2;
+    }
+    for (int j4 = 64; j4 < degA; j4 += 4) {
         int idx = j4 + e;
-        bool val = idx < deg;
-        unsigned s = val ? csr_src[beg + idx] : (unsigned)i;
+        bool val = idx < degA;
+        unsigned s = val ? csr_src[begA + idx] : (unsigned)iA;
         if (act) {
             float aw = isgat ? as2[s] : nrm[s];
             float w;
-            if (isgat) {
-                w = val ? __expf(leakyf(aw + adv)) : 0.f;
-                sumw += w;
-            } else {
-                w = val ? aw * ni : 0.f;
-            }
+            if (isgat) { w = val ? __expf(leakyf(aw + advA)) : 0.f; sumwA += w; }
+            else       { w = val ? aw * niA : 0.f; }
             uint4 hv = hgv[(size_t)s * 10 + c];
             float2 p0 = unpack2_bf16(hv.x), p1 = unpack2_bf16(hv.y);
             float2 p2 = unpack2_bf16(hv.z), p3 = unpack2_bf16(hv.w);
-            acc[0] = fmaf(p0.x, w, acc[0]); acc[1] = fmaf(p0.y, w, acc[1]);
-            acc[2] = fmaf(p1.x, w, acc[2]); acc[3] = fmaf(p1.y, w, acc[3]);
-            acc[4] = fmaf(p2.x, w, acc[4]); acc[5] = fmaf(p2.y, w, acc[5]);
-            acc[6] = fmaf(p3.x, w, acc[6]); acc[7] = fmaf(p3.y, w, acc[7]);
+            accA[0] = fmaf(p0.x, w, accA[0]); accA[1] = fmaf(p0.y, w, accA[1]);
+            accA[2] = fmaf(p1.x, w, accA[2]); accA[3] = fmaf(p1.y, w, accA[3]);
+            accA[4] = fmaf(p2.x, w, accA[4]); accA[5] = fmaf(p2.y, w, accA[5]);
+            accA[6] = fmaf(p3.x, w, accA[6]); accA[7] = fmaf(p3.y, w, accA[7]);
+        }
+    }
+    for (int j4 = 64; j4 < degB; j4 += 4) {
+        int idx = j4 + e;
+        bool val = idx < degB;
+        unsigned s = val ? csr_src[begB + idx] : (unsigned)iBs;
+        if (act) {
+            float aw = isgat ? as2[s] : nrm[s];
+            float w;
+            if (isgat) { w = val ? __expf(leakyf(aw + advB)) : 0.f; sumwB += w; }
+            else       { w = val ? aw * niB : 0.f; }
+            uint4 hv = hgv[(size_t)s * 10 + c];
+            float2 p0 = unpack2_bf16(hv.x), p1 = unpack2_bf16(hv.y);
+            float2 p2 = unpack2_bf16(hv.z), p3 = unpack2_bf16(hv.w);
+            accB[0] = fmaf(p0.x, w, accB[0]); accB[1] = fmaf(p0.y, w, accB[1]);
+            accB[2] = fmaf(p1.x, w, accB[2]); accB[3] = fmaf(p1.y, w, accB[3]);
+            accB[4] = fmaf(p2.x, w, accB[4]); accB[5] = fmaf(p2.y, w, accB[5]);
+            accB[6] = fmaf(p3.x, w, accB[6]); accB[7] = fmaf(p3.y, w, accB[7]);
         }
     }
 
 #pragma unroll
     for (int t = 0; t < 8; ++t) {
-        acc[t] += __shfl_xor(acc[t], 1, 64);
-        acc[t] += __shfl_xor(acc[t], 2, 64);
-    }
-    sumw += __shfl_xor(sumw, 1, 64);
-    sumw += __shfl_xor(sumw, 2, 64);
-    const float ssum = sumw + eself;
-
-    if (act && e == 0) {
-        if (isgat) {
-            float inv = 1.f / ssum, wt = *wt_p;
-            float4 b0 = *(const float4*)&gat_b2[c * 8];
-            float4 b1 = *(const float4*)&gat_b2[c * 8 + 4];
-            float4 o0 = make_float4((acc[0] * inv + b0.x) * wt, (acc[1] * inv + b0.y) * wt,
-                                    (acc[2] * inv + b0.z) * wt, (acc[3] * inv + b0.w) * wt);
-            float4 o1 = make_float4((acc[4] * inv + b1.x) * wt, (acc[5] * inv + b1.y) * wt,
-                                    (acc[6] * inv + b1.z) * wt, (acc[7] * inv + b1.w) * wt);
-            *(float4*)&cat[(size_t)i * 80 + 40 + c * 8]     = o0;
-            *(float4*)&cat[(size_t)i * 80 + 40 + c * 8 + 4] = o1;
-        } else {
-            float wc = *wc_p;
-            int g = c - 5;
-            float4 b0 = *(const float4*)&gcn_b2[g * 8];
-            float4 b1 = *(const float4*)&gcn_b2[g * 8 + 4];
-            float4 o0 = make_float4((acc[0] + b0.x) * wc, (acc[1] + b0.y) * wc,
-                                    (acc[2] + b0.z) * wc, (acc[3] + b0.w) * wc);
-            float4 o1 = make_float4((acc[4] + b1.x) * wc, (acc[5] + b1.y) * wc,
-                                    (acc[6] + b1.z) * wc, (acc[7] + b1.w) * wc);
-            *(float4*)&cat[(size_t)i * 80 + g * 8]     = o0;
-            *(float4*)&cat[(size_t)i * 80 + g * 8 + 4] = o1;
-        }
+        accA[t] += __shfl_xor(accA[t], 1, 64); accA[t] += __shfl_xor(accA[t], 2, 64);
+        accB[t] += __shfl_xor(accB[t], 1, 64); accB[t] += __shfl_xor(accB[t], 2, 64);
+    }
+    sumwA += __shfl_xor(sumwA, 1, 64); sumwA += __shfl_xor(sumwA, 2, 64);
+    sumwB += __shfl_xor(sumwB, 1, 64); sumwB += __shfl_xor(sumwB, 2, 64);
+
+    const float invA = 1.f / (sumwA + eselfA);
+    const float invB = 1.f / (sumwB + eselfB);
+    const float wtv = *wt_p, wcv = *wc_p;
+    float cvA[8], cvB[8];
+#pragma unroll
+    for (int t = 0; t < 8; ++t) { cvA[t] = 0.f; cvB[t] = 0.f; }
+    if (isgat) {
+        float4 b0 = *(const float4*)&gat_b2[c * 8];
+        float4 b1 = *(const float4*)&gat_b2[c * 8 + 4];
+        float bb[8] = {b0.x, b0.y, b0.z, b0.w, b1.x, b1.y, b1.z, b1.w};
+#pragma unroll
+        for (int t = 0; t < 8; ++t) {
+            cvA[t] = (accA[t] * invA + bb[t]) * wtv;
+            cvB[t] = (accB[t] * invB + bb[t]) * wtv;
+        }
+    } else if (act) {
+        float4 b0 = *(const float4*)&gcn_b2[(c - 5) * 8];
+        float4 b1 = *(const float4*)&gcn_b2[(c - 5) * 8 + 4];
+        float bb[8] = {b0.x, b0.y, b0.z, b0.w, b1.x, b1.y, b1.z, b1.w};
+#pragma unroll
+        for (int t = 0; t < 8; ++t) {
+            cvA[t] = (accA[t] + bb[t]) * wcv;
+            cvB[t] = (accB[t] + bb[t]) * wcv;
+        }
+    }
+
+    const int oc = lane < 40 ? lane : 0;
+    const float lb = lin_b[oc];
+    float oA = lb, oB = lb;
+#pragma unroll
+    for (int kc = 0; kc < 10; ++kc) {
+        const int srcl = 4 * (kc < 5 ? 5 + kc : kc - 5);
+        float4 w0 = *(const float4*)&Wt[oc * 84 + kc * 8];
+        float4 w1 = *(const float4*)&Wt[oc * 84 + kc * 8 + 4];
+        float wv[8] = {w0.x, w0.y, w0.z, w0.w, w1.x, w1.y, w1.z, w1.w};
+#pragma unroll
+        for (int t = 0; t < 8; ++t) {
+            float ca = __shfl(cvA[t], srcl, 64);
+            float cb = __shfl(cvB[t], srcl, 64);
+            oA = fmaf(ca, wv[t], oA);
+            oB = fmaf(cb, wv[t], oB);
+        }
+    }
+    if (lane < 40) {
+        Y[(size_t)iA * 40 + lane] = oA;
+        if (hasB) Y[(size_t)iB * 40 + lane] = oB;
     }
 }
 
@@ -835,18 +958,17 @@
     float* ad1     = (float*)alloc((size_t)n * 4 * 4);
     float* as2     = (float*)alloc((size_t)n * 4);
     float* ad2     = (float*)alloc((size_t)n * 4);
-    float* cat     = (float*)alloc((size_t)n * 80 * 4);
+    unsigned* hb   = (unsigned*)alloc((size_t)n * 80 * 4);
     unsigned* hg_b = (unsigned*)alloc((size_t)n * 40 * 4);
     float* xg      = (float*)alloc((size_t)n * F_IN * 4);
     unsigned* gaccb= (unsigned*)alloc((size_t)n * 16 * 4);
-    unsigned* bpair = (unsigned*)cat;
+    unsigned* bpair = hb;
     uint2*    ovf   = (uint2*)(bpair + (size_t)NBUCK * BCAP);
-    unsigned* hb    = (unsigned*)cat;
     unsigned* xgb   = (unsigned*)xg;
     unsigned* ovf_cnt = bcnt + NBUCK;
 
     const int NB = (n + 255) / 256;
-    const int WB = (n + 3) / 4;
+    const int WB2 = (n + 7) / 8;
     const int SB = (e + SCHUNK - 1) / SCHUNK;
 
     hipMemsetAsync(bcnt, 0, (size_t)(NBUCK + 1) * 4, stream);
@@ -862,15 +984,14 @@
     gemm1_mfma_kernel<<<(n + 63) / 64, 256, 0, stream>>>(x, wbf, att_s1, att_d1,
                                                          hb, as1, ad1, n);
 
-    agg1_fused_kernel<<<WB, 256, 0, stream>>>(hb, as1, ad1, nrm, rs, csr_src,
-                                              gat_b1, gcn_b1, xgb, gaccb, n);
+    agg1_fused_kernel<<<WB2, 256, 0, stream>>>(hb, as1, ad1, nrm, rs, csr_src,
+                                               gat_b1, gcn_b1, xgb, gaccb, n);
 
     gemm_tile_bb<32, 40, 128, 32, 40, 20><<<(n + 127) / 128, 320, 0, stream>>>(gaccb, gcn_W2, hg_b, n);
     gemm2_gat_kernel<<<(n + 127) / 128, 320, 0, stream>>>(xgb, gat_W2, att_s2, att_d2,
                                                           hg_b, as2, ad2, n);
 
-    agg2_fused_kernel<<<WB, 256, 0, stream>>>(hg_b, as2, ad2, nrm, rs, csr_src,
-                                              gat_b2, gcn_b2, wc_p, wt_p, cat, n);
-
-    gemm_tile<80, 40, 128, 40><<<(n + 127) / 128, 320, 0, stream>>>(cat, lin_W, lin_b, (float*)d_out, n);
-}
+    agg2_fused_kernel<<<WB2, 256, 0, stream>>>(hg_b, as2, ad2, nrm, rs, csr_src,
+                                               gat_b2, gcn_b2, wc_p, wt_p,
+                                               lin_W, lin_b, (float*)d_out, n);
+}
```

Result: slower. 403.8 us (+31.9%).
